# Kernel tuning notes

Hardware: AMD Instinct MI355X
Metric: run time of the kernel (lower is better)

The kernel has to match this reference:

```python
import jax, jax.numpy as jnp
import numpy as np


def _highway(x, Ws, bs):
    # Ws: [n_hw, 2H, H] (torch Linear layout), bs: [n_hw, 2H]
    H = x.shape[-1]
    for i in range(Ws.shape[0]):
        proj = jnp.einsum('bsh,oh->bso', x, Ws[i]) + bs[i]
        nonlin = jax.nn.relu(proj[..., :H])
        gate = jax.nn.sigmoid(proj[..., H:])
        x = gate * x + (1.0 - gate) * nonlin
    return x


def setup_inputs() -> dict:
    key = jax.random.key(0)
    ks = jax.random.split(key, 10)
    B, S, H, L, W, NHW = 32, 512, 512, 2, 4, 2
    scale = 1.0 / np.sqrt(H)
    return {
        'inputs': jax.random.normal(ks[0], (B, S, H), dtype=jnp.float32),
        'masks': jnp.ones((B, S), dtype=jnp.int32),
        'fwd_pads': jax.random.normal(ks[1], (L, W, H), dtype=jnp.float32) * scale,
        'bwd_pads': jax.random.normal(ks[2], (L, W, H), dtype=jnp.float32) * scale,
        'fwd_ws': jax.random.normal(ks[3], (L, W + 1), dtype=jnp.float32),
        'bwd_ws': jax.random.normal(ks[4], (L, W + 1), dtype=jnp.float32),
        'fwd_hw_W': jax.random.normal(ks[5], (L, NHW, 2 * H, H), dtype=jnp.float32) * scale,
        'fwd_hw_b': jax.random.normal(ks[6], (L, NHW, 2 * H), dtype=jnp.float32) * 0.1,
        'bwd_hw_W': jax.random.normal(ks[7], (L, NHW, 2 * H, H), dtype=jnp.float32) * scale,
        'bwd_hw_b': jax.random.normal(ks[8], (L, NHW, 2 * H), dtype=jnp.float32) * 0.1,
    }


def reference(inputs, masks, fwd_pads, bwd_pads, fwd_ws, bwd_ws,
              fwd_hw_W, fwd_hw_b, bwd_hw_W, bwd_hw_b):
    # inputs: [B,S,H]; masks unused (as in the torch module)
    B, S, H = inputs.shape
    L, W, _ = fwd_pads.shape
    fwd_in = inputs
    bwd_in = inputs
    outs = []
    for l in range(L):
        fp = jnp.broadcast_to(fwd_pads[l], (B, W, H))
        bp = jnp.broadcast_to(bwd_pads[l], (B, W, H))
        pf = jnp.concatenate([fp, fwd_in, bp], axis=1)  # [B, S+2W, H]
        pb = jnp.concatenate([fp, bwd_in, bp], axis=1)
        # forward window at t covers padded positions t..t+W (causal)
        f_win = jnp.stack([pf[:, k:k + S] for k in range(W + 1)], axis=0)  # [W+1,B,S,H]
        f_out = jnp.einsum('k,kbsh->bsh', fwd_ws[l], f_win)
        # backward window at t covers padded positions t+W..t+2W (anti-causal)
        b_win = jnp.stack([pb[:, W + k:W + k + S] for k in range(W + 1)], axis=0)
        b_out = jnp.einsum('k,kbsh->bsh', bwd_ws[l], b_win)
        f_out = _highway(f_out, fwd_hw_W[l], fwd_hw_b[l])
        b_out = _highway(b_out, bwd_hw_W[l], bwd_hw_b[l])
        fwd_in, bwd_in = f_out, b_out
        outs.append(jnp.concatenate([f_out, b_out], axis=-1))
    return jnp.stack(outs, axis=0)  # [L, B, S, 2H]
```

## Files before the change

### kernel.cpp

```cpp
#include <hip/hip_runtime.h>
#include <hip/hip_bf16.h>

typedef __attribute__((ext_vector_type(8))) short bf16x8;
typedef __attribute__((ext_vector_type(4))) float floatx4;

#define B_ 32
#define S_ 512
#define H_ 512
#define M_ (B_*S_)
#define K_ 512
#define N_ 1024

__device__ __forceinline__ void gload_lds16(const void* g, void* l) {
  __builtin_amdgcn_global_load_lds(
      (const __attribute__((address_space(1))) void*)g,
      (__attribute__((address_space(3))) void*)l, 16, 0, 0);
}

__global__ void cvt_kernel(const float* __restrict__ src,
                           __hip_bfloat16* __restrict__ dst, int n4) {
  int t = blockIdx.x * 256 + threadIdx.x;
  if (t >= n4) return;
  float4 v = *(const float4*)(src + (size_t)t * 4);
  union { ushort4 u; __hip_bfloat16 h[4]; } pk;
  pk.h[0] = __float2bfloat16(v.x);
  pk.h[1] = __float2bfloat16(v.y);
  pk.h[2] = __float2bfloat16(v.z);
  pk.h[3] = __float2bfloat16(v.w);
  *(ushort4*)((unsigned short*)dst + (size_t)t * 4) = pk.u;
}

__global__ void conv_kernel(const float* __restrict__ inf, const float* __restrict__ inb,
                            int instride,
                            const float* __restrict__ fpad, const float* __restrict__ bpad,
                            const float* __restrict__ fw, const float* __restrict__ bw,
                            __hip_bfloat16* __restrict__ xaf, __hip_bfloat16* __restrict__ xab) {
  int t = blockIdx.x * 256 + threadIdx.x;
  int dir = blockIdx.y;
  int row = t >> 7;
  int hv  = (t & 127) << 2;
  int s = row & (S_ - 1);
  float4 a = make_float4(0.f, 0.f, 0.f, 0.f);
  if (dir == 0) {
#pragma unroll
    for (int k = 0; k < 5; ++k) {
      float w = fw[k];
      const float* src = (s + k < 4) ? (fpad + (size_t)(s + k) * H_ + hv)
                                     : (inf + (size_t)(row + k - 4) * instride + hv);
      float4 v = *(const float4*)src;
      a.x += w * v.x; a.y += w * v.y; a.z += w * v.z; a.w += w * v.w;
    }
  } else {
#pragma unroll
    for (int k = 0; k < 5; ++k) {
      float w = bw[k];
      const float* src = (s + k < S_) ? (inb + (size_t)(row + k) * instride + hv)
                                      : (bpad + (size_t)(s + k - S_) * H_ + hv);
      float4 v = *(const float4*)src;
      a.x += w * v.x; a.y += w * v.y; a.z += w * v.z; a.w += w * v.w;
    }
  }
  __hip_bfloat16* xa = dir ? xab : xaf;
  union { ushort4 u; __hip_bfloat16 h[4]; } pk;
  pk.h[0] = __float2bfloat16(a.x);
  pk.h[1] = __float2bfloat16(a.y);
  pk.h[2] = __float2bfloat16(a.z);
  pk.h[3] = __float2bfloat16(a.w);
  *(ushort4*)((unsigned short*)xa + (size_t)row * H_ + hv) = pk.u;
}

__global__ void hw_gemm(const __hip_bfloat16* __restrict__ Af, const __hip_bfloat16* __restrict__ Ab,
                        const __hip_bfloat16* __restrict__ Wf, const __hip_bfloat16* __restrict__ Wb,
                        const float* __restrict__ biasf, const float* __restrict__ biasb,
                        __hip_bfloat16* __restrict__ Anf, __hip_bfloat16* __restrict__ Anb,
                        float* __restrict__ outp, int final_mode) {
  __shared__ __align__(16) char smem[32768];
  __hip_bfloat16* lA = (__hip_bfloat16*)smem;
  __hip_bfloat16* lB = (__hip_bfloat16*)(smem + 16384);

  const int tid = threadIdx.x;
  const int lane = tid & 63, wave = tid >> 6;
  const int wm = wave >> 1, wn = wave & 1;
  const int quad = lane >> 4, l16 = lane & 15;
  const int dir = blockIdx.z;

  const int n = blockIdx.y * 8 + blockIdx.x;
  const int xcd = n & 7;
  const int h0 = ((n >> 3) & 7) * 64;
  const int m0 = (xcd + (n >> 6) * 8) * 128;

  const __hip_bfloat16* A = dir ? Ab : Af;
  const __hip_bfloat16* Wm = dir ? Wb : Wf;
  const float* bias = dir ? biasb : biasf;
  __hip_bfloat16* An = dir ? Anb : Anf;

  floatx4 acc[4][4];
#pragma unroll
  for (int i = 0; i < 4; ++i)
#pragma unroll
    for (int j = 0; j < 4; ++j) acc[i][j] = (floatx4){0.f, 0.f, 0.f, 0.f};

  float xs[4][2][4];

  const int srow = lane >> 3;
  const int skk  = (((lane & 7) ^ srow) << 3);
  const int xkp  = h0 >> 6;
  const int sw   = l16 & 7;

  const __hip_bfloat16* aptr[4];
  const __hip_bfloat16* bptr[4];
#pragma unroll
  for (int c = 0; c < 4; ++c) {
    const int chunk = wave * 4 + c;
    const int arow = chunk * 8 + srow;
    aptr[c] = A + (size_t)(m0 + arow) * K_ + skk;
    const int brow = chunk * 8 + srow;
    const int wrow = (brow < 64) ? (h0 + brow) : (512 + h0 + brow - 64);
    bptr[c] = Wm + (size_t)wrow * K_ + skk;
  }

  for (int kp = 0; kp < 8; ++kp) {
    const int kb = kp * 64;
#pragma unroll
    for (int c = 0; c < 4; ++c) {
      const int chunk = wave * 4 + c;
      gload_lds16(aptr[c] + kb, &lA[chunk * 512]);
      gload_lds16(bptr[c] + kb, &lB[chunk * 512]);
    }
    __syncthreads();

    if (kp == xkp) {
#pragma unroll
      for (int i = 0; i < 4; ++i)
#pragma unroll
        for (int j = 0; j < 2; ++j)
#pragma unroll
          for (int r = 0; r < 4; ++r) {
            const int ra = wm * 64 + i * 16 + quad * 4 + r;
            const int c2 = wn * 32 + j * 16 + l16;
            xs[i][j][r] = __bfloat162float(
                lA[ra * 64 + ((((c2 >> 3) ^ (ra & 7)) << 3) | (c2 & 7))]);
          }
    }

#pragma unroll
    for (int ks = 0; ks < 2; ++ks) {
      bf16x8 av[4], bv[4];
#pragma unroll
      for (int i = 0; i < 4; ++i) {
        const int ra = wm * 64 + i * 16 + l16;
        av[i] = *(const bf16x8*)&lA[ra * 64 + (((ks * 4 + quad) ^ sw) << 3)];
      }
#pragma unroll
      for (int j = 0; j < 2; ++j) {
        const int rb = wn * 32 + j * 16 + l16;
        bv[j] = *(const bf16x8*)&lB[rb * 64 + (((ks * 4 + quad) ^ sw) << 3)];
      }
#pragma unroll
      for (int j = 0; j < 2; ++j) {
        const int rb = 64 + wn * 32 + j * 16 + l16;
        bv[2 + j] = *(const bf16x8*)&lB[rb * 64 + (((ks * 4 + quad) ^ sw) << 3)];
      }
#pragma unroll
      for (int i = 0; i < 4; ++i)
#pragma unroll
        for (int j = 0; j < 4; ++j)
          acc[i][j] = __builtin_amdgcn_mfma_f32_16x16x32_bf16(av[i], bv[j], acc[i][j], 0, 0, 0);
    }
    __syncthreads();
  }

  const int cbase = h0 + wn * 32 + l16;
  const int cloc = wn * 32 + l16;
  float bnl[2], bgt[2];
#pragma unroll
  for (int j = 0; j < 2; ++j) {
    bnl[j] = bias[cbase + j * 16];
    bgt[j] = bias[512 + cbase + j * 16];
  }

  if (final_mode) {
    float* ft = (float*)smem;
#pragma unroll
    for (int i = 0; i < 4; ++i) {
      const int rb = wm * 64 + i * 16 + quad * 4;
#pragma unroll
      for (int r = 0; r < 4; ++r) {
#pragma unroll
        for (int j = 0; j < 2; ++j) {
          float pn = acc[i][j][r] + bnl[j];
          float pg = acc[i][j + 2][r] + bgt[j];
          float g = 1.f / (1.f + __expf(-pg));
          float xo = xs[i][j][r];
          ft[(rb + r) * 64 + cloc + j * 16] = g * xo + (1.f - g) * fmaxf(pn, 0.f);
        }
      }
    }
    __syncthreads();
    const float* src = (const float*)smem;
#pragma unroll
    for (int p = 0; p < 8; ++p) {
      const int rl = p * 16 + (tid >> 4);
      const int cc = (tid & 15) * 4;
      float4 v = *(const float4*)&src[rl * 64 + cc];
      *(float4*)&outp[(size_t)(m0 + rl) * N_ + dir * H_ + h0 + cc] = v;
    }
  } else {
    __hip_bfloat16* bt = (__hip_bfloat16*)smem;
#pragma unroll
    for (int i = 0; i < 4; ++i) {
      const int rb = wm * 64 + i * 16 + quad * 4;
#pragma unroll
      for (int r = 0; r < 4; ++r) {
#pragma unroll
        for (int j = 0; j < 2; ++j) {
          float pn = acc[i][j][r] + bnl[j];
          float pg = acc[i][j + 2][r] + bgt[j];
          float g = 1.f / (1.f + __expf(-pg));
          float xo = xs[i][j][r];
          bt[(rb + r) * 64 + cloc + j * 16] =
              __float2bfloat16(g * xo + (1.f - g) * fmaxf(pn, 0.f));
        }
      }
    }
    __syncthreads();
    const unsigned short* src = (const unsigned short*)smem;
#pragma unroll
    for (int p = 0; p < 4; ++p) {
      const int rl = p * 32 + (tid >> 3);
      const int cc = (tid & 7) * 8;
      int4 v = *(const int4*)(src + rl * 64 + cc);
      *(int4*)((unsigned short*)An + (size_t)(m0 + rl) * H_ + h0 + cc) = v;
    }
  }
}

extern "C" void kernel_launch(void* const* d_in, const int* in_sizes, int n_in,
                              void* d_out, int out_size, void* d_ws, size_t ws_size,
                              hipStream_t stream) {
  const float* inputs   = (const float*)d_in[0];
  const float* fwd_pads = (const float*)d_in[2];
  const float* bwd_pads = (const float*)d_in[3];
  const float* fwd_ws_p = (const float*)d_in[4];
  const float* bwd_ws_p = (const float*)d_in[5];
  const float* fwd_hw_W = (const float*)d_in[6];
  const float* fwd_hw_b = (const float*)d_in[7];
  const float* bwd_hw_W = (const float*)d_in[8];
  const float* bwd_hw_b = (const float*)d_in[9];
  float* out = (float*)d_out;

  char* ws = (char*)d_ws;
  size_t off = 0;
  __hip_bfloat16* Wbf = (__hip_bfloat16*)(ws + off); off += (size_t)4194304 * 2;
  __hip_bfloat16* xa0f = (__hip_bfloat16*)(ws + off); off += (size_t)M_ * H_ * 2;
  __hip_bfloat16* xa0b = (__hip_bfloat16*)(ws + off); off += (size_t)M_ * H_ * 2;
  __hip_bfloat16* xa1f = (__hip_bfloat16*)(ws + off); off += (size_t)M_ * H_ * 2;
  __hip_bfloat16* xa1b = (__hip_bfloat16*)(ws + off); off += (size_t)M_ * H_ * 2;

  cvt_kernel<<<2048, 256, 0, stream>>>(fwd_hw_W, Wbf, 524288);
  cvt_kernel<<<2048, 256, 0, stream>>>(bwd_hw_W, Wbf + (size_t)2097152, 524288);

  for (int l = 0; l < 2; ++l) {
    const float *inf, *inb;
    int instride;
    if (l == 0) { inf = inputs; inb = inputs; instride = H_; }
    else        { inf = out;    inb = out + H_; instride = N_; }
    conv_kernel<<<dim3(8192, 2), 256, 0, stream>>>(
        inf, inb, instride,
        fwd_pads + (size_t)l * 4 * H_, bwd_pads + (size_t)l * 4 * H_,
        fwd_ws_p + l * 5, bwd_ws_p + l * 5,
        xa0f, xa0b);

    hw_gemm<<<dim3(8, 128, 2), 256, 0, stream>>>(
        xa0f, xa0b,
        Wbf + (size_t)(l * 2) * 524288, Wbf + (size_t)2097152 + (size_t)(l * 2) * 524288,
        fwd_hw_b + (l * 2) * 1024, bwd_hw_b + (l * 2) * 1024,
        xa1f, xa1b, nullptr, 0);

    hw_gemm<<<dim3(8, 128, 2), 256, 0, stream>>>(
        xa1f, xa1b,
        Wbf + (size_t)(l * 2 + 1) * 524288, Wbf + (size_t)2097152 + (size_t)(l * 2 + 1) * 524288,
        fwd_hw_b + (l * 2 + 1) * 1024, bwd_hw_b + (l * 2 + 1) * 1024,
        nullptr, nullptr, out + (size_t)l * M_ * N_, 1);
  }
}
```

Measured before the change: 480.6 us.

## Enlarge highway GEMM tiles to 256x256 with double-buffered LDS K-loop

Rewrites the fused highway GEMM to use 512-thread blocks computing 256 rows by 128 output columns (256 weight rows including gate), with K-step 32 and double-buffered LDS so the next tile's global-to-LDS loads overlap the current MFMAs. The skip-connection x values are kept as packed bf16 pairs to save registers, and the grid drops to 512 blocks. This aims to raise arithmetic intensity and hide load latency, at the cost of more registers and 64KB LDS, which reduces occupancy, and fewer blocks than before.

```diff
diff --git a/kernel.cpp b/kernel.cpp
--- a/kernel.cpp
+++ b/kernel.cpp
@@ -69,14 +69,13 @@
   *(ushort4*)((unsigned short*)xa + (size_t)row * H_ + hv) = pk.u;
 }
 
-__global__ void hw_gemm(const __hip_bfloat16* __restrict__ Af, const __hip_bfloat16* __restrict__ Ab,
-                        const __hip_bfloat16* __restrict__ Wf, const __hip_bfloat16* __restrict__ Wb,
-                        const float* __restrict__ biasf, const float* __restrict__ biasb,
-                        __hip_bfloat16* __restrict__ Anf, __hip_bfloat16* __restrict__ Anb,
-                        float* __restrict__ outp, int final_mode) {
-  __shared__ __align__(16) char smem[32768];
-  __hip_bfloat16* lA = (__hip_bfloat16*)smem;
-  __hip_bfloat16* lB = (__hip_bfloat16*)(smem + 16384);
+__global__ __launch_bounds__(512, 2)
+void hw_gemm(const __hip_bfloat16* __restrict__ Af, const __hip_bfloat16* __restrict__ Ab,
+             const __hip_bfloat16* __restrict__ Wf, const __hip_bfloat16* __restrict__ Wb,
+             const float* __restrict__ biasf, const float* __restrict__ biasb,
+             __hip_bfloat16* __restrict__ Anf, __hip_bfloat16* __restrict__ Anb,
+             float* __restrict__ outp, int final_mode) {
+  __shared__ __align__(16) char smem[65536];
 
   const int tid = threadIdx.x;
   const int lane = tid & 63, wave = tid >> 6;
@@ -84,152 +83,187 @@
   const int quad = lane >> 4, l16 = lane & 15;
   const int dir = blockIdx.z;
 
-  const int n = blockIdx.y * 8 + blockIdx.x;
-  const int xcd = n & 7;
-  const int h0 = ((n >> 3) & 7) * 64;
-  const int m0 = (xcd + (n >> 6) * 8) * 128;
+  const int n = blockIdx.x;
+  const int by = n & 63, bx = n >> 6;
+  const int m0 = by * 256;
+  const int h0 = bx * 128;
 
   const __hip_bfloat16* A = dir ? Ab : Af;
   const __hip_bfloat16* Wm = dir ? Wb : Wf;
   const float* bias = dir ? biasb : biasf;
   __hip_bfloat16* An = dir ? Anb : Anf;
 
-  floatx4 acc[4][4];
+  floatx4 acc[4][8];
 #pragma unroll
   for (int i = 0; i < 4; ++i)
 #pragma unroll
-    for (int j = 0; j < 4; ++j) acc[i][j] = (floatx4){0.f, 0.f, 0.f, 0.f};
-
-  float xs[4][2][4];
-
-  const int srow = lane >> 3;
-  const int skk  = (((lane & 7) ^ srow) << 3);
-  const int xkp  = h0 >> 6;
-  const int sw   = l16 & 7;
-
-  const __hip_bfloat16* aptr[4];
-  const __hip_bfloat16* bptr[4];
-#pragma unroll
-  for (int c = 0; c < 4; ++c) {
-    const int chunk = wave * 4 + c;
-    const int arow = chunk * 8 + srow;
-    aptr[c] = A + (size_t)(m0 + arow) * K_ + skk;
-    const int brow = chunk * 8 + srow;
-    const int wrow = (brow < 64) ? (h0 + brow) : (512 + h0 + brow - 64);
+    for (int j = 0; j < 8; ++j) acc[i][j] = (floatx4){0.f, 0.f, 0.f, 0.f};
+
+  const int srow = lane >> 2;
+  const int skk  = (((lane & 3) ^ ((lane >> 3) & 3)) << 3);
+  const int key  = (l16 >> 1) & 3;
+  const int xkp0 = bx * 4 + wn * 2;
+  const int xkp1 = xkp0 + 1;
+
+  const __hip_bfloat16* aptr[2];
+  const __hip_bfloat16* bptr[2];
+#pragma unroll
+  for (int c = 0; c < 2; ++c) {
+    const int chunk = wave * 2 + c;
+    aptr[c] = A + (size_t)(m0 + chunk * 16 + srow) * K_ + skk;
+    const int brow = chunk * 16 + srow;
+    const int wnp = brow >> 7, rr = brow & 127;
+    const int wrow = (rr < 64) ? (h0 + wnp * 64 + rr)
+                               : (512 + h0 + wnp * 64 + (rr - 64));
     bptr[c] = Wm + (size_t)wrow * K_ + skk;
   }
 
-  for (int kp = 0; kp < 8; ++kp) {
-    const int kb = kp * 64;
-#pragma unroll
-    for (int c = 0; c < 4; ++c) {
-      const int chunk = wave * 4 + c;
-      gload_lds16(aptr[c] + kb, &lA[chunk * 512]);
-      gload_lds16(bptr[c] + kb, &lB[chunk * 512]);
+#pragma unroll
+  for (int c = 0; c < 2; ++c) {
+    const int chunk = wave * 2 + c;
+    gload_lds16(aptr[c], smem + chunk * 1024);
+    gload_lds16(bptr[c], smem + 16384 + chunk * 1024);
+  }
+  __syncthreads();
+
+  unsigned int xsp[4][4][2];
+  int cur = 0;
+  for (int kp = 0; kp < 16; ++kp) {
+    const __hip_bfloat16* cA = (const __hip_bfloat16*)(smem + (cur << 15));
+    const __hip_bfloat16* cB = (const __hip_bfloat16*)(smem + (cur << 15) + 16384);
+    if (kp < 15) {
+      char* nb = smem + ((cur ^ 1) << 15);
+      const int kb = (kp + 1) * 32;
+#pragma unroll
+      for (int c = 0; c < 2; ++c) {
+        const int chunk = wave * 2 + c;
+        gload_lds16(aptr[c] + kb, nb + chunk * 1024);
+        gload_lds16(bptr[c] + kb, nb + 16384 + chunk * 1024);
+      }
+    }
+    if (kp == xkp0) {
+      const unsigned short* pA = (const unsigned short*)cA;
+#pragma unroll
+      for (int i = 0; i < 4; ++i)
+#pragma unroll
+        for (int jj = 0; jj < 2; ++jj)
+#pragma unroll
+          for (int rh = 0; rh < 2; ++rh) {
+            const int ra0 = wm * 64 + i * 16 + quad * 4 + rh * 2;
+            const int ra1 = ra0 + 1;
+            const int c2 = jj * 16 + l16;
+            unsigned int lo = pA[ra0 * 32 + ((((c2 >> 3) ^ ((ra0 >> 1) & 3)) << 3) | (c2 & 7))];
+            unsigned int hi = pA[ra1 * 32 + ((((c2 >> 3) ^ ((ra1 >> 1) & 3)) << 3) | (c2 & 7))];
+            xsp[i][jj][rh] = lo | (hi << 16);
+          }
+    }
+    if (kp == xkp1) {
+      const unsigned short* pA = (const unsigned short*)cA;
+#pragma unroll
+      for (int i = 0; i < 4; ++i)
+#pragma unroll
+        for (int jj = 0; jj < 2; ++jj)
+#pragma unroll
+          for (int rh = 0; rh < 2; ++rh) {
+            const int ra0 = wm * 64 + i * 16 + quad * 4 + rh * 2;
+            const int ra1 = ra0 + 1;
+            const int c2 = jj * 16 + l16;
+            unsigned int lo = pA[ra0 * 32 + ((((c2 >> 3) ^ ((ra0 >> 1) & 3)) << 3) | (c2 & 7))];
+            unsigned int hi = pA[ra1 * 32 + ((((c2 >> 3) ^ ((ra1 >> 1) & 3)) << 3) | (c2 & 7))];
+            xsp[i][2 + jj][rh] = lo | (hi << 16);
+          }
+    }
+    bf16x8 av[4];
+#pragma unroll
+    for (int i = 0; i < 4; ++i) {
+      const int ra = wm * 64 + i * 16 + l16;
+      av[i] = *(const bf16x8*)&cA[ra * 32 + ((quad ^ key) << 3)];
+    }
+#pragma unroll
+    for (int jh = 0; jh < 2; ++jh) {
+      bf16x8 bv[4];
+#pragma unroll
+      for (int jj = 0; jj < 4; ++jj) {
+        const int rb = wn * 128 + (jh * 4 + jj) * 16 + l16;
+        bv[jj] = *(const bf16x8*)&cB[rb * 32 + ((quad ^ key) << 3)];
+      }
+#pragma unroll
+      for (int i = 0; i < 4; ++i)
+#pragma unroll
+        for (int jj = 0; jj < 4; ++jj)
+          acc[i][jh * 4 + jj] =
+              __builtin_amdgcn_mfma_f32_16x16x32_bf16(av[i], bv[jj], acc[i][jh * 4 + jj], 0, 0, 0);
     }
     __syncthreads();
-
-    if (kp == xkp) {
-#pragma unroll
-      for (int i = 0; i < 4; ++i)
-#pragma unroll
-        for (int j = 0; j < 2; ++j)
-#pragma unroll
-          for (int r = 0; r < 4; ++r) {
-            const int ra = wm * 64 + i * 16 + quad * 4 + r;
-            const int c2 = wn * 32 + j * 16 + l16;
-            xs[i][j][r] = __bfloat162float(
-                lA[ra * 64 + ((((c2 >> 3) ^ (ra & 7)) << 3) | (c2 & 7))]);
-          }
-    }
-
-#pragma unroll
-    for (int ks = 0; ks < 2; ++ks) {
-      bf16x8 av[4], bv[4];
-#pragma unroll
-      for (int i = 0; i < 4; ++i) {
-        const int ra = wm * 64 + i * 16 + l16;
-        av[i] = *(const bf16x8*)&lA[ra * 64 + (((ks * 4 + quad) ^ sw) << 3)];
-      }
-#pragma unroll
-      for (int j = 0; j < 2; ++j) {
-        const int rb = wn * 32 + j * 16 + l16;
-        bv[j] = *(const bf16x8*)&lB[rb * 64 + (((ks * 4 + quad) ^ sw) << 3)];
-      }
-#pragma unroll
-      for (int j = 0; j < 2; ++j) {
-        const int rb = 64 + wn * 32 + j * 16 + l16;
-        bv[2 + j] = *(const bf16x8*)&lB[rb * 64 + (((ks * 4 + quad) ^ sw) << 3)];
-      }
-#pragma unroll
-      for (int i = 0; i < 4; ++i)
-#pragma unroll
-        for (int j = 0; j < 4; ++j)
-          acc[i][j] = __builtin_amdgcn_mfma_f32_16x16x32_bf16(av[i], bv[j], acc[i][j], 0, 0, 0);
-    }
-    __syncthreads();
-  }
-
-  const int cbase = h0 + wn * 32 + l16;
-  const int cloc = wn * 32 + l16;
-  float bnl[2], bgt[2];
-#pragma unroll
-  for (int j = 0; j < 2; ++j) {
-    bnl[j] = bias[cbase + j * 16];
-    bgt[j] = bias[512 + cbase + j * 16];
+    cur ^= 1;
+  }
+
+  float bnl[4], bgt[4];
+#pragma unroll
+  for (int j = 0; j < 4; ++j) {
+    const int c = h0 + wn * 64 + j * 16 + l16;
+    bnl[j] = bias[c];
+    bgt[j] = bias[512 + c];
   }
 
   if (final_mode) {
     float* ft = (float*)smem;
 #pragma unroll
-    for (int i = 0; i < 4; ++i) {
-      const int rb = wm * 64 + i * 16 + quad * 4;
-#pragma unroll
-      for (int r = 0; r < 4; ++r) {
-#pragma unroll
-        for (int j = 0; j < 2; ++j) {
-          float pn = acc[i][j][r] + bnl[j];
-          float pg = acc[i][j + 2][r] + bgt[j];
-          float g = 1.f / (1.f + __expf(-pg));
-          float xo = xs[i][j][r];
-          ft[(rb + r) * 64 + cloc + j * 16] = g * xo + (1.f - g) * fmaxf(pn, 0.f);
-        }
-      }
-    }
-    __syncthreads();
-    const float* src = (const float*)smem;
-#pragma unroll
-    for (int p = 0; p < 8; ++p) {
-      const int rl = p * 16 + (tid >> 4);
-      const int cc = (tid & 15) * 4;
-      float4 v = *(const float4*)&src[rl * 64 + cc];
-      *(float4*)&outp[(size_t)(m0 + rl) * N_ + dir * H_ + h0 + cc] = v;
+    for (int p = 0; p < 2; ++p) {
+      if (wn == p) {
+#pragma unroll
+        for (int i = 0; i < 4; ++i)
+#pragma unroll
+          for (int r = 0; r < 4; ++r) {
+            const int rl = wm * 64 + i * 16 + quad * 4 + r;
+#pragma unroll
+            for (int j = 0; j < 4; ++j) {
+              float pn = acc[i][j][r] + bnl[j];
+              float pg = acc[i][j + 4][r] + bgt[j];
+              float g = 1.f / (1.f + __expf(-pg));
+              unsigned int u = xsp[i][j][r >> 1];
+              unsigned int bits = (r & 1) ? (u >> 16) : (u & 0xffffu);
+              float xo = __uint_as_float(bits << 16);
+              ft[rl * 64 + j * 16 + l16] = g * xo + (1.f - g) * fmaxf(pn, 0.f);
+            }
+          }
+      }
+      __syncthreads();
+#pragma unroll
+      for (int q = 0; q < 8; ++q) {
+        const int rl = q * 32 + (tid >> 4);
+        const int cc = (tid & 15) * 4;
+        float4 v = *(const float4*)&ft[rl * 64 + cc];
+        *(float4*)&outp[(size_t)(m0 + rl) * N_ + dir * H_ + h0 + p * 64 + cc] = v;
+      }
+      __syncthreads();
     }
   } else {
     __hip_bfloat16* bt = (__hip_bfloat16*)smem;
 #pragma unroll
-    for (int i = 0; i < 4; ++i) {
-      const int rb = wm * 64 + i * 16 + quad * 4;
+    for (int i = 0; i < 4; ++i)
 #pragma unroll
       for (int r = 0; r < 4; ++r) {
-#pragma unroll
-        for (int j = 0; j < 2; ++j) {
+        const int rl = wm * 64 + i * 16 + quad * 4 + r;
+#pragma unroll
+        for (int j = 0; j < 4; ++j) {
           float pn = acc[i][j][r] + bnl[j];
-          float pg = acc[i][j + 2][r] + bgt[j];
+          float pg = acc[i][j + 4][r] + bgt[j];
           float g = 1.f / (1.f + __expf(-pg));
-          float xo = xs[i][j][r];
-          bt[(rb + r) * 64 + cloc + j * 16] =
+          unsigned int u = xsp[i][j][r >> 1];
+          unsigned int bits = (r & 1) ? (u >> 16) : (u & 0xffffu);
+          float xo = __uint_as_float(bits << 16);
+          bt[rl * 128 + wn * 64 + j * 16 + l16] =
               __float2bfloat16(g * xo + (1.f - g) * fmaxf(pn, 0.f));
         }
       }
-    }
     __syncthreads();
     const unsigned short* src = (const unsigned short*)smem;
 #pragma unroll
-    for (int p = 0; p < 4; ++p) {
-      const int rl = p * 32 + (tid >> 3);
-      const int cc = (tid & 7) * 8;
-      int4 v = *(const int4*)(src + rl * 64 + cc);
+    for (int p = 0; p < 8; ++p) {
+      const int rl = p * 32 + (tid >> 4);
+      const int cc = (tid & 15) * 8;
+      int4 v = *(const int4*)(src + rl * 128 + cc);
       *(int4*)((unsigned short*)An + (size_t)(m0 + rl) * H_ + h0 + cc) = v;
     }
   }
@@ -271,13 +305,13 @@
         fwd_ws_p + l * 5, bwd_ws_p + l * 5,
         xa0f, xa0b);
 
-    hw_gemm<<<dim3(8, 128, 2), 256, 0, stream>>>(
+    hw_gemm<<<dim3(256, 1, 2), 512, 0, stream>>>(
         xa0f, xa0b,
         Wbf + (size_t)(l * 2) * 524288, Wbf + (size_t)2097152 + (size_t)(l * 2) * 524288,
         fwd_hw_b + (l * 2) * 1024, bwd_hw_b + (l * 2) * 1024,
         xa1f, xa1b, nullptr, 0);
 
-    hw_gemm<<<dim3(8, 128, 2), 256, 0, stream>>>(
+    hw_gemm<<<dim3(256, 1, 2), 512, 0, stream>>>(
         xa1f, xa1b,
         Wbf + (size_t)(l * 2 + 1) * 524288, Wbf + (size_t)2097152 + (size_t)(l * 2 + 1) * 524288,
         fwd_hw_b + (l * 2 + 1) * 1024, bwd_hw_b + (l * 2 + 1) * 1024,
```

Result: faster. 422.4 us (-12.1%).
